# Kernel tuning notes

Hardware: AMD Instinct MI355X
Metric: run time of the kernel (lower is better)

Reference implementation:

```python
import jax, jax.numpy as jnp
import numpy as np

SMOOTH = 1e-5
ALPHA = 0.25
GAMMA = 2.0
INIT_BETA = 0.5
BETA_DECAY = 0.99


def setup_inputs() -> dict:
    key = jax.random.key(0)
    ks = jax.random.split(key, 7)
    B, NC, C, H, W, D = 8, 1000, 19, 512, 512, 768
    return {
        "logits": jax.random.normal(ks[0], (B, NC), dtype=jnp.float32),
        "label": jax.random.randint(ks[1], (B,), 0, NC),
        "vision_feat": jax.random.normal(ks[2], (B, D), dtype=jnp.float32),
        "text_feat": jax.random.normal(ks[3], (B, D), dtype=jnp.float32),
        "modal_mask": jax.random.uniform(ks[4], (B, 2), dtype=jnp.float32),
        "seg_mask": jax.random.normal(ks[5], (B, C, H, W), dtype=jnp.float32),
        "seg_gt": jax.random.randint(ks[6], (B, H, W), 0, C),
        "epoch": 5,
    }


def _ce_mean(logits, label):
    logp = jax.nn.log_softmax(logits, axis=-1)
    return -jnp.take_along_axis(logp, label[:, None], axis=-1).mean()


def _dice_loss(pred, target):
    # pred: [B,C,H,W] (raw, as in the torch module), target: [B,H,W] int
    C = pred.shape[1]
    onehot = (target[:, None, :, :] == jnp.arange(C)[None, :, None, None]).astype(pred.dtype)
    inter = jnp.sum(pred * onehot, axis=(2, 3))          # [B,C]
    union = jnp.sum(pred, axis=(2, 3)) + jnp.sum(onehot, axis=(2, 3))
    dice = (2.0 * inter + SMOOTH) / (union + SMOOTH)
    return jnp.mean(1.0 - dice)


def _focal_loss(pred, target):
    # pred: [B,C,H,W] logits over class axis 1
    logp = jax.nn.log_softmax(pred, axis=1)
    logp_t = jnp.take_along_axis(logp, target[:, None, :, :], axis=1)[:, 0]  # [B,H,W]
    p_t = jnp.exp(logp_t)
    ce = -logp_t
    return jnp.mean(ALPHA * (1.0 - p_t) ** GAMMA * ce)


def _modal_balance(vision_feat, text_feat, modal_mask, epoch):
    beta_t = INIT_BETA * BETA_DECAY ** epoch
    vn = vision_feat / jnp.linalg.norm(vision_feat, axis=1, keepdims=True)
    tn = text_feat / jnp.linalg.norm(text_feat, axis=1, keepdims=True)
    v_cons = jnp.mean((vn - vn.mean(axis=0, keepdims=True)) ** 2)
    t_cons = jnp.mean((tn - tn.mean(axis=0, keepdims=True)) ** 2)
    cross = 1.0 - jnp.mean(jnp.sum(vn * tn, axis=1))  # cosine sim of unit vectors
    return ((1.0 - beta_t) * v_cons * modal_mask[:, 0].mean()
            + beta_t * t_cons * modal_mask[:, 1].mean() + cross)


def reference(logits, label, vision_feat, text_feat, modal_mask, seg_mask, seg_gt, epoch):
    ce = _ce_mean(logits, label)
    mb = _modal_balance(vision_feat, text_feat, modal_mask, epoch)
    seg = _dice_loss(seg_mask, seg_gt) + _focal_loss(seg_mask, seg_gt)
    total = ce + 0.3 * mb + 0.5 * seg
    return total
```

## Files before the change

### kernel.cpp

```cpp
#include <hip/hip_runtime.h>
#include <math.h>

#define SMOOTH_F 1e-5f
#define ALPHA_F 0.25f

constexpr int Bn = 8;
constexpr int NCn = 1000;
constexpr int Cn = 19;
constexpr int HWn = 512 * 512;
constexpr int Dn = 768;
constexpr int BC = Bn * Cn;

constexpr int TPB = 256;
constexpr int G4 = HWn / 4;
constexpr int BLKS_PER_B = G4 / TPB;
constexpr int SEG_BLOCKS = Bn * BLKS_PER_B;

constexpr int PLANE = SEG_BLOCKS;
constexpr int NPLANES = 3 * Cn + 1;
constexpr int WS_CE = NPLANES * PLANE;
constexpr int WS_MB = WS_CE + 1;

__device__ __forceinline__ float wave_sum(float v) {
#pragma unroll
  for (int off = 32; off > 0; off >>= 1) v += __shfl_down(v, off, 64);
  return v;
}
__device__ __forceinline__ float wave_max(float v) {
#pragma unroll
  for (int off = 32; off > 0; off >>= 1) v = fmaxf(v, __shfl_down(v, off, 64));
  return v;
}

__global__ __launch_bounds__(TPB, 2) void k_seg(
    const float* __restrict__ pred, const int* __restrict__ gt,
    const float* __restrict__ logits, const int* __restrict__ label,
    const float* __restrict__ vf, const float* __restrict__ tf,
    const float* __restrict__ mmask, const int* __restrict__ epoch,
    float* __restrict__ ws) {
  __shared__ float s_inter[Cn];
  __shared__ float s_count[Cn];
  __shared__ float s_pred[Cn];
  __shared__ float s_red[4];
  __shared__ float sA[4];
  __shared__ float sBv[4];
  __shared__ float nv[Bn];
  __shared__ float nt[Bn];

  const int tid = threadIdx.x;
  const int wid = tid >> 6, lane = tid & 63;
  const int blk = blockIdx.x;

  if (blk >= SEG_BLOCKS) {
    if (blk == SEG_BLOCKS) {
      float acc = 0.0f;
      for (int b = 0; b < Bn; ++b) {
        const float* row = logits + b * NCn;
        float lm = -INFINITY;
        for (int j = tid; j < NCn; j += TPB) lm = fmaxf(lm, row[j]);
        lm = wave_max(lm);
        if (lane == 0) sA[wid] = lm;
        __syncthreads();
        float bm = fmaxf(fmaxf(sA[0], sA[1]), fmaxf(sA[2], sA[3]));
        __syncthreads();
        float ls = 0.0f;
        for (int j = tid; j < NCn; j += TPB) ls += expf(row[j] - bm);
        ls = wave_sum(ls);
        if (lane == 0) sA[wid] = ls;
        __syncthreads();
        if (tid == 0) {
          float lse = bm + logf(sA[0] + sA[1] + sA[2] + sA[3]);
          acc += row[label[b]] - lse;
        }
        __syncthreads();
      }
      if (tid == 0) ws[WS_CE] = -(acc / (float)Bn);
    } else {
      for (int b = 0; b < Bn; ++b) {
        float sv = 0.0f, st = 0.0f;
        for (int j = tid; j < Dn; j += TPB) {
          float a = vf[b * Dn + j];
          float c = tf[b * Dn + j];
          sv += a * a;
          st += c * c;
        }
        sv = wave_sum(sv);
        st = wave_sum(st);
        if (lane == 0) { sA[wid] = sv; sBv[wid] = st; }
        __syncthreads();
        if (tid == 0) {
          nv[b] = sqrtf(sA[0] + sA[1] + sA[2] + sA[3]);
          nt[b] = sqrtf(sBv[0] + sBv[1] + sBv[2] + sBv[3]);
        }
        __syncthreads();
      }
      float colv = 0.0f, colt = 0.0f, cross = 0.0f;
      for (int j = tid; j < Dn; j += TPB) {
        float sv = 0.0f, ssv = 0.0f, stt = 0.0f, sst = 0.0f, cr = 0.0f;
        for (int b = 0; b < Bn; ++b) {
          float vn = vf[b * Dn + j] / nv[b];
          float tn = tf[b * Dn + j] / nt[b];
          sv += vn; ssv += vn * vn;
          stt += tn; sst += tn * tn;
          cr += vn * tn;
        }
        colv += ssv - sv * sv * 0.125f;
        colt += sst - stt * stt * 0.125f;
        cross += cr;
      }
      colv = wave_sum(colv);
      colt = wave_sum(colt);
      cross = wave_sum(cross);
      if (lane == 0) { sA[wid] = colv; sBv[wid] = colt; s_red[wid] = cross; }
      __syncthreads();
      if (tid == 0) {
        float cv = sA[0] + sA[1] + sA[2] + sA[3];
        float ct = sBv[0] + sBv[1] + sBv[2] + sBv[3];
        float cr = s_red[0] + s_red[1] + s_red[2] + s_red[3];
        float v_cons = cv / (float)(Bn * Dn);
        float t_cons = ct / (float)(Bn * Dn);
        float crossv = 1.0f - cr * 0.125f;
        float beta = 0.5f * powf(0.99f, (float)epoch[0]);
        float mm0 = 0.0f, mm1 = 0.0f;
        for (int b = 0; b < Bn; ++b) { mm0 += mmask[b * 2]; mm1 += mmask[b * 2 + 1]; }
        mm0 *= 0.125f; mm1 *= 0.125f;
        ws[WS_MB] = (1.0f - beta) * v_cons * mm0 + beta * t_cons * mm1 + crossv;
      }
    }
    return;
  }

  const int b = blk >> 8;
  const int grp = ((blk & 255) << 8) + tid;

  const float4* pred4 = (const float4*)pred + (size_t)b * Cn * G4 + grp;
  const int4 t4 = ((const int4*)gt)[(size_t)b * G4 + grp];
  float4 x[Cn];
#pragma unroll
  for (int c = 0; c < Cn; ++c) x[c] = pred4[(size_t)c * G4];
#pragma unroll
  for (int c = 0; c < Cn; ++c)
    asm volatile("" : "+v"(x[c].x), "+v"(x[c].y), "+v"(x[c].z), "+v"(x[c].w));

  if (tid < Cn) { s_inter[tid] = 0.0f; s_count[tid] = 0.0f; s_pred[tid] = 0.0f; }
  __syncthreads();

  float focal = 0.0f;
#pragma unroll
  for (int j = 0; j < 4; ++j) {
    const int t = (j == 0) ? t4.x : (j == 1) ? t4.y : (j == 2) ? t4.z : t4.w;
    float m = (j == 0) ? x[0].x : (j == 1) ? x[0].y : (j == 2) ? x[0].z : x[0].w;
#pragma unroll
    for (int c = 1; c < Cn; ++c) {
      const float v = (j == 0) ? x[c].x : (j == 1) ? x[c].y : (j == 2) ? x[c].z : x[c].w;
      m = fmaxf(m, v);
    }
    float se = 0.0f, xt = 0.0f;
#pragma unroll
    for (int c = 0; c < Cn; ++c) {
      const float v = (j == 0) ? x[c].x : (j == 1) ? x[c].y : (j == 2) ? x[c].z : x[c].w;
      se += expf(v - m);
      if (t == c) xt = v;
    }
    const float lse = m + logf(se);
    const float lpt = xt - lse;
    const float p = expf(lpt);
    const float om = 1.0f - p;
    focal += om * om * (-lpt);
    atomicAdd(&s_inter[t], xt);
    atomicAdd(&s_count[t], 1.0f);
  }

#pragma unroll
  for (int c = 0; c < Cn; ++c) {
    float pc = x[c].x + x[c].y + x[c].z + x[c].w;
    pc = wave_sum(pc);
    if (lane == 0) atomicAdd(&s_pred[c], pc);
  }
  const float fw = wave_sum(focal * ALPHA_F);
  if (lane == 0) s_red[wid] = fw;
  __syncthreads();

  if (tid < Cn) {
    ws[(size_t)tid * PLANE + blk] = s_inter[tid];
    ws[(size_t)(Cn + tid) * PLANE + blk] = s_pred[tid];
    ws[(size_t)(2 * Cn + tid) * PLANE + blk] = s_count[tid];
  }
  if (tid == 0)
    ws[(size_t)(3 * Cn) * PLANE + blk] = s_red[0] + s_red[1] + s_red[2] + s_red[3];
}

__global__ __launch_bounds__(1024) void k_final(
    const float* __restrict__ ws, float* __restrict__ out) {
  __shared__ float s_part[912];
  __shared__ float s_d[3];
  __shared__ float s_f;
  const int tid = threadIdx.x;
  const int wid = tid >> 6, lane = tid & 63;

  if (tid < 2 * 3 * BC) {
    const int job = tid >> 1;
    const int half = tid & 1;
    const int quant = job / BC;
    const int pair = job - quant * BC;
    const int b = pair / Cn;
    const int c = pair - b * Cn;
    const float4* p = (const float4*)(ws + (size_t)(quant * Cn + c) * PLANE +
                                      b * 256 + half * 128);
    float s = 0.0f;
#pragma unroll 8
    for (int k = 0; k < 32; ++k) {
      const float4 v = p[k];
      s += v.x + v.y + v.z + v.w;
    }
    s_part[tid] = s;
  }
  if (wid == 15) {
    const float4* p = (const float4*)(ws + (size_t)(3 * Cn) * PLANE) + lane * 8;
    float f = 0.0f;
#pragma unroll
    for (int k = 0; k < 8; ++k) {
      const float4 v = p[k];
      f += v.x + v.y + v.z + v.w;
    }
    f = wave_sum(f);
    if (lane == 0) s_f = f;
  }
  __syncthreads();

  float v = 0.0f;
  if (tid < BC) {
    const float inter = s_part[(0 * BC + tid) * 2] + s_part[(0 * BC + tid) * 2 + 1];
    const float ps    = s_part[(1 * BC + tid) * 2] + s_part[(1 * BC + tid) * 2 + 1];
    const float cnt   = s_part[(2 * BC + tid) * 2] + s_part[(2 * BC + tid) * 2 + 1];
    const float dice = (2.0f * inter + SMOOTH_F) / (ps + cnt + SMOOTH_F);
    v = 1.0f - dice;
  }
  v = wave_sum(v);
  if (lane == 0 && wid < 3) s_d[wid] = v;
  __syncthreads();

  if (tid == 0) {
    const float dice_mean = (s_d[0] + s_d[1] + s_d[2]) / (float)BC;
    const float focal_mean = s_f / (float)(Bn * HWn);
    const float seg = dice_mean + focal_mean;
    out[0] = ws[WS_CE] + 0.3f * ws[WS_MB] + 0.5f * seg;
  }
}

extern "C" void kernel_launch(void* const* d_in, const int* in_sizes, int n_in,
                              void* d_out, int out_size, void* d_ws, size_t ws_size,
                              hipStream_t stream) {
  const float* logits = (const float*)d_in[0];
  const int* label    = (const int*)d_in[1];
  const float* vf     = (const float*)d_in[2];
  const float* tf     = (const float*)d_in[3];
  const float* mmask  = (const float*)d_in[4];
  const float* seg    = (const float*)d_in[5];
  const int* gt       = (const int*)d_in[6];
  const int* epoch    = (const int*)d_in[7];
  float* out = (float*)d_out;
  float* ws = (float*)d_ws;

  hipLaunchKernelGGL(k_seg, dim3(SEG_BLOCKS + 2), dim3(TPB), 0, stream,
                     seg, gt, logits, label, vf, tf, mmask, epoch, ws);
  hipLaunchKernelGGL(k_final, dim3(1), dim3(1024), 0, stream, ws, out);
}
```

Baseline: 267.9 us.

## Stream seg loads with single-pass unshifted softmax and raise occupancy

Measured after the change: 260.6 us. 2.7% less time.

```diff
diff --git a/kernel.cpp b/kernel.cpp
--- a/kernel.cpp
+++ b/kernel.cpp
@@ -32,7 +32,7 @@
   return v;
 }
 
-__global__ __launch_bounds__(TPB, 2) void k_seg(
+__global__ __launch_bounds__(TPB, 4) void k_seg(
     const float* __restrict__ pred, const int* __restrict__ gt,
     const float* __restrict__ logits, const int* __restrict__ label,
     const float* __restrict__ vf, const float* __restrict__ tf,
@@ -51,8 +51,8 @@
   const int wid = tid >> 6, lane = tid & 63;
   const int blk = blockIdx.x;
 
-  if (blk >= SEG_BLOCKS) {
-    if (blk == SEG_BLOCKS) {
+  if (blk < 2) {
+    if (blk == 0) {
       float acc = 0.0f;
       for (int b = 0; b < Bn; ++b) {
         const float* row = logits + b * NCn;
@@ -130,51 +130,50 @@
     return;
   }
 
-  const int b = blk >> 8;
-  const int grp = ((blk & 255) << 8) + tid;
+  const int sblk = blk - 2;
+  const int b = sblk >> 8;
+  const int grp = ((sblk & 255) << 8) + tid;
 
   const float4* pred4 = (const float4*)pred + (size_t)b * Cn * G4 + grp;
   const int4 t4 = ((const int4*)gt)[(size_t)b * G4 + grp];
-  float4 x[Cn];
-#pragma unroll
-  for (int c = 0; c < Cn; ++c) x[c] = pred4[(size_t)c * G4];
-#pragma unroll
-  for (int c = 0; c < Cn; ++c)
-    asm volatile("" : "+v"(x[c].x), "+v"(x[c].y), "+v"(x[c].z), "+v"(x[c].w));
 
   if (tid < Cn) { s_inter[tid] = 0.0f; s_count[tid] = 0.0f; s_pred[tid] = 0.0f; }
   __syncthreads();
 
+  float4 se = make_float4(0.0f, 0.0f, 0.0f, 0.0f);
+  float4 xt = make_float4(0.0f, 0.0f, 0.0f, 0.0f);
+  float psum[Cn];
+#pragma unroll
+  for (int c = 0; c < Cn; ++c) {
+    const float4 v = pred4[(size_t)c * G4];
+    psum[c] = v.x + v.y + v.z + v.w;
+    se.x += __expf(v.x);
+    se.y += __expf(v.y);
+    se.z += __expf(v.z);
+    se.w += __expf(v.w);
+    if (t4.x == c) xt.x = v.x;
+    if (t4.y == c) xt.y = v.y;
+    if (t4.z == c) xt.z = v.z;
+    if (t4.w == c) xt.w = v.w;
+  }
+
   float focal = 0.0f;
 #pragma unroll
   for (int j = 0; j < 4; ++j) {
-    const int t = (j == 0) ? t4.x : (j == 1) ? t4.y : (j == 2) ? t4.z : t4.w;
-    float m = (j == 0) ? x[0].x : (j == 1) ? x[0].y : (j == 2) ? x[0].z : x[0].w;
-#pragma unroll
-    for (int c = 1; c < Cn; ++c) {
-      const float v = (j == 0) ? x[c].x : (j == 1) ? x[c].y : (j == 2) ? x[c].z : x[c].w;
-      m = fmaxf(m, v);
-    }
-    float se = 0.0f, xt = 0.0f;
-#pragma unroll
-    for (int c = 0; c < Cn; ++c) {
-      const float v = (j == 0) ? x[c].x : (j == 1) ? x[c].y : (j == 2) ? x[c].z : x[c].w;
-      se += expf(v - m);
-      if (t == c) xt = v;
-    }
-    const float lse = m + logf(se);
-    const float lpt = xt - lse;
-    const float p = expf(lpt);
+    const float sej = (j == 0) ? se.x : (j == 1) ? se.y : (j == 2) ? se.z : se.w;
+    const float xtj = (j == 0) ? xt.x : (j == 1) ? xt.y : (j == 2) ? xt.z : xt.w;
+    const int t     = (j == 0) ? t4.x : (j == 1) ? t4.y : (j == 2) ? t4.z : t4.w;
+    const float lpt = xtj - __logf(sej);
+    const float p = __expf(lpt);
     const float om = 1.0f - p;
     focal += om * om * (-lpt);
-    atomicAdd(&s_inter[t], xt);
+    atomicAdd(&s_inter[t], xtj);
     atomicAdd(&s_count[t], 1.0f);
   }
 
 #pragma unroll
   for (int c = 0; c < Cn; ++c) {
-    float pc = x[c].x + x[c].y + x[c].z + x[c].w;
-    pc = wave_sum(pc);
+    float pc = wave_sum(psum[c]);
     if (lane == 0) atomicAdd(&s_pred[c], pc);
   }
   const float fw = wave_sum(focal * ALPHA_F);
@@ -182,12 +181,12 @@
   __syncthreads();
 
   if (tid < Cn) {
-    ws[(size_t)tid * PLANE + blk] = s_inter[tid];
-    ws[(size_t)(Cn + tid) * PLANE + blk] = s_pred[tid];
-    ws[(size_t)(2 * Cn + tid) * PLANE + blk] = s_count[tid];
+    ws[(size_t)tid * PLANE + sblk] = s_inter[tid];
+    ws[(size_t)(Cn + tid) * PLANE + sblk] = s_pred[tid];
+    ws[(size_t)(2 * Cn + tid) * PLANE + sblk] = s_count[tid];
   }
   if (tid == 0)
-    ws[(size_t)(3 * Cn) * PLANE + blk] = s_red[0] + s_red[1] + s_red[2] + s_red[3];
+    ws[(size_t)(3 * Cn) * PLANE + sblk] = s_red[0] + s_red[1] + s_red[2] + s_red[3];
 }
 
 __global__ __launch_bounds__(1024) void k_final(
```
